# Kernel optimization log

Measured on AMD Instinct MI355X. Metric: run time of the kernel, lower is better.

Reference implementation:

```python
import jax, jax.numpy as jnp
import numpy as np

B, S, I, HS = 256, 512, 64, 128


def setup_inputs() -> dict:
    key = jax.random.key(0)
    ks = jax.random.split(key, 5)
    def xavier(k, shape):
        fan_in, fan_out = shape
        lim = float(np.sqrt(6.0 / (fan_in + fan_out)))
        return jax.random.uniform(k, shape, jnp.float32, -lim, lim)
    return {
        "x": jax.random.normal(ks[0], (B, S, I), jnp.float32),
        "TimeDiff": jax.random.uniform(ks[1], (B, S, I), jnp.float32),
        "weights_x": xavier(ks[2], (I, 5 * HS)),
        "weights_h": xavier(ks[3], (HS, 3 * HS)),
        "weights_t": xavier(ks[4], (I, 3 * HS)),
        "bias": jnp.zeros((5 * HS,), jnp.float32),
    }


def _time_lstm(x, TimeDiff, weights_x, weights_h, weights_t, bias):
    hs = weights_h.shape[0]
    bs = x.shape[0]
    # the original clamps weights_t[:, :HS] to max=0 in-place every step;
    # clamping once up front is equivalent.
    wt = weights_t.at[:, :hs].set(jnp.minimum(weights_t[:, :hs], 0.0))
    # precompute input-dependent projections for the whole sequence
    gx = jnp.einsum('bsi,ih->bsh', x, weights_x)        # (B,S,5H)
    gt = jnp.einsum('bsi,ih->bsh', TimeDiff, wt)         # (B,S,3H)

    b0, b1, b2, b3, b4 = (bias[:hs], bias[hs:2*hs], bias[2*hs:3*hs],
                          bias[3*hs:4*hs], bias[4*hs:])

    def step(carry, inp):
        h, c = carry
        gx_t, gt_t = inp                                  # (B,5H), (B,3H)
        xh = h @ weights_h                                # (B,3H)
        i_t = jax.nn.sigmoid(gx_t[:, :hs] + xh[:, :hs] + b0)
        t1 = jax.nn.sigmoid(gx_t[:, hs:2*hs] + jnp.tanh(gt_t[:, :hs]) + b1)
        t2 = jax.nn.sigmoid(gx_t[:, 2*hs:3*hs] + jnp.tanh(gt_t[:, hs:2*hs]) + b2)
        cwa = jnp.tanh(gx_t[:, 3*hs:4*hs] + xh[:, hs:2*hs] + b3)
        c_tilde = jax.nn.sigmoid((1.0 - i_t * t1) * c + i_t * t1 * cwa)
        c_new = jax.nn.sigmoid((1.0 - i_t) * c + i_t * t2 * cwa)
        o_t = jax.nn.sigmoid(gx_t[:, 4*hs:] + gt_t[:, 2*hs:] + xh[:, 2*hs:] + b4)
        h_new = o_t + jnp.tanh(c_tilde)
        return (h_new, c_new), h_new

    h0 = jnp.zeros((bs, hs), x.dtype)
    c0 = jnp.zeros((bs, hs), x.dtype)
    # scan over time: (S,B,*)
    (h_f, c_f), hseq = jax.lax.scan(
        step, (h0, c0),
        (jnp.swapaxes(gx, 0, 1), jnp.swapaxes(gt, 0, 1)))
    hidden_seq = jnp.swapaxes(hseq, 0, 1)                 # (B,S,H)
    return hidden_seq, (h_f, c_f)


def reference(x, TimeDiff, weights_x, weights_h, weights_t, bias):
    return _time_lstm(x, TimeDiff, weights_x, weights_h, weights_t, bias)
```

## Files before the change

kernel.cpp:

```cpp
#include <hip/hip_runtime.h>

typedef unsigned short ushort_t;
typedef unsigned int uint_t;
typedef short short8 __attribute__((ext_vector_type(8)));
typedef float f32x4 __attribute__((ext_vector_type(4)));
typedef uint_t u32x2 __attribute__((ext_vector_type(2)));
typedef _Float16 half2_t __attribute__((ext_vector_type(2)));

__device__ __forceinline__ float sigm(float x) { return 1.f / (1.f + __expf(-x)); }
__device__ __forceinline__ float tanh_s(float x) {
  float e = __expf(2.f * fabsf(x));
  float r = 1.f - 2.f / (e + 1.f);
  return copysignf(r, x);
}
__device__ __forceinline__ float dot2h(half2_t a, half2_t b, float c) {
#if __has_builtin(__builtin_amdgcn_fdot2)
  return __builtin_amdgcn_fdot2(a, b, c, false);
#else
  return c + (float)a.x * (float)b.x + (float)a.y * (float)b.y;
#endif
}
__device__ __forceinline__ uint_t cvtpk_bf16(float a, float b) {
  uint_t r;
  asm("v_cvt_pk_bf16_f32 %0, %1, %2" : "=v"(r) : "v"(a), "v"(b));
  return r;
}
__device__ __forceinline__ short8 ld_cvt8(const float* p) {
  f32x4 v0 = *(const f32x4*)p;
  f32x4 v1 = *(const f32x4*)(p + 4);
  union { short8 s; uint_t u[4]; } r;
  r.u[0] = cvtpk_bf16(v0[0], v0[1]);
  r.u[1] = cvtpk_bf16(v0[2], v0[3]);
  r.u[2] = cvtpk_bf16(v1[0], v1[1]);
  r.u[3] = cvtpk_bf16(v1[2], v1[3]);
  return r.s;
}
__device__ __forceinline__ float f16b2f(uint_t bits) {
  union { ushort_t s; _Float16 h; } v; v.s = (ushort_t)bits; return (float)v.h;
}
__device__ __forceinline__ uint_t f2f16b(float f) {
  union { _Float16 h; ushort_t s; } v; v.h = (_Float16)f; return v.s;
}

#define MFMAB(a, b, c) __builtin_amdgcn_mfma_f32_16x16x32_bf16((a), (b), (c), 0, 0, 0)

__global__ __launch_bounds__(512) void gemm_g(
    const float* __restrict__ x, const float* __restrict__ td,
    const float* __restrict__ wx, const float* __restrict__ wt,
    const float* __restrict__ bias, u32x2* __restrict__ G,
    int t0, int TC, int ltc, int rpt)
{
  const int tid = threadIdx.x;
  const int wv = tid >> 6, lane = tid & 63;
  const int l15 = lane & 15, lg = lane >> 4;
  const int jj = wv * 16 + l15;

  short8 Bx[5][2], Bt[3][2];
#pragma unroll
  for (int s = 0; s < 5; ++s)
#pragma unroll
    for (int f = 0; f < 2; ++f) {
      const float* wp = wx + (size_t)(f * 32 + lg * 8) * 640 + s * 128 + jj;
      union { short8 v; uint_t u[4]; } r;
#pragma unroll
      for (int q = 0; q < 4; ++q)
        r.u[q] = cvtpk_bf16(wp[(2 * q) * 640], wp[(2 * q + 1) * 640]);
      Bx[s][f] = r.v;
    }
#pragma unroll
  for (int s = 0; s < 3; ++s)
#pragma unroll
    for (int f = 0; f < 2; ++f) {
      const float* wp = wt + (size_t)(f * 32 + lg * 8) * 384 + s * 128 + jj;
      union { short8 v; uint_t u[4]; } r;
#pragma unroll
      for (int q = 0; q < 4; ++q) {
        float w0 = wp[(2 * q) * 384], w1 = wp[(2 * q + 1) * 384];
        if (s == 0) { w0 = fminf(w0, 0.f); w1 = fminf(w1, 0.f); }
        r.u[q] = cvtpk_bf16(w0, w1);
      }
      Bt[s][f] = r.v;
    }

  const float b0f = bias[jj], b1f = bias[128 + jj], b2f = bias[256 + jj];
  const float b3f = bias[384 + jj], b4f = bias[512 + jj];

#pragma unroll 1
  for (int it = 0; it < rpt; ++it) {
    const int m0 = (blockIdx.x * rpt + it) * 16;
    const int m = m0 + l15;
    const int bb = m >> ltc, tt = m & (TC - 1);
    const size_t ro = ((size_t)(bb * 512) + t0 + tt) * 64 + lg * 8;
    short8 xa0 = ld_cvt8(x + ro), xa1 = ld_cvt8(x + ro + 32);
    short8 ta0 = ld_cvt8(td + ro), ta1 = ld_cvt8(td + ro + 32);

    f32x4 g0{}, g1{}, g2{}, g3{}, g4{}, q0{}, q1{}, q2{};
    g0 = MFMAB(xa0, Bx[0][0], g0); g0 = MFMAB(xa1, Bx[0][1], g0);
    g1 = MFMAB(xa0, Bx[1][0], g1); g1 = MFMAB(xa1, Bx[1][1], g1);
    g2 = MFMAB(xa0, Bx[2][0], g2); g2 = MFMAB(xa1, Bx[2][1], g2);
    g3 = MFMAB(xa0, Bx[3][0], g3); g3 = MFMAB(xa1, Bx[3][1], g3);
    g4 = MFMAB(xa0, Bx[4][0], g4); g4 = MFMAB(xa1, Bx[4][1], g4);
    q0 = MFMAB(ta0, Bt[0][0], q0); q0 = MFMAB(ta1, Bt[0][1], q0);
    q1 = MFMAB(ta0, Bt[1][0], q1); q1 = MFMAB(ta1, Bt[1][1], q1);
    q2 = MFMAB(ta0, Bt[2][0], q2); q2 = MFMAB(ta1, Bt[2][1], q2);

#pragma unroll
    for (int r = 0; r < 4; ++r) {
      float v0 = g0[r] + b0f;
      float T1 = sigm(g1[r] + b1f + tanh_s(q0[r]));
      float T2 = sigm(g2[r] + b2f + tanh_s(q1[r]));
      float v3 = g3[r] + b3f;
      float v4 = g4[r] + b4f + q2[r];
      uint_t t1u = (uint_t)(T1 * 255.f + 0.5f);
      uint_t t2u = (uint_t)(T2 * 255.f + 0.5f);
      u32x2 P;
      P[0] = f2f16b(v0) | (f2f16b(v3) << 16);
      P[1] = f2f16b(v4) | (t1u << 16) | (t2u << 24);
      G[(size_t)(m0 + lg * 4 + r) * 128 + jj] = P;
    }
  }
}

__global__ __launch_bounds__(768) void scan_k(
    const u32x2* __restrict__ G, const float* __restrict__ wh,
    float* __restrict__ out, float* __restrict__ sh, float* __restrict__ sc,
    int t0, int t1, int TC)
{
  __shared__ __attribute__((aligned(16))) _Float16 h_lds[128];
  __shared__ float xh_lds[768];
  const int tid = threadIdx.x;
  const int b = blockIdx.x;
  const int half = (tid >= 384) ? 1 : 0;
  const int j = tid - half * 384;

  half2_t w2[32];
  {
    const float* wp = wh + (size_t)(half * 64) * 384 + j;
#pragma unroll
    for (int k = 0; k < 32; ++k)
      w2[k] = half2_t{(_Float16)wp[(2 * k) * 384], (_Float16)wp[(2 * k + 1) * 384]};
  }

  float c_last = 0.f, h0v = 0.f;
  if (tid < 128) {
    if (t0 > 0) { h0v = sh[b * 128 + tid]; c_last = sc[b * 128 + tid]; }
    h_lds[tid] = (_Float16)h0v;
  }
  float h_last = h0v;

  const u32x2* Gp = G + (size_t)b * TC * 128 + (tid & 127);
  float* outp = out + (size_t)b * 65536 + tid;

  u32x2 p0{}, p1{}, p2{}, p3{};
  if (tid < 128) {
    p0 = Gp[0];
    p1 = Gp[128];
    p2 = Gp[256];
    p3 = Gp[384];
  }
  __syncthreads();

#define SCAN_STEP(P, TABS)                                                   \
  {                                                                          \
       \
    u32x2 cur = P;                                                           \
    if (tid < 128) {                                                         \
      int ldr = (TABS) - t0 + 4; if (ldr > TC - 1) ldr = TC - 1;             \
      P = Gp[(size_t)ldr * 128];                                             \
    }                                                                        \
    float a0 = 0.f, a1 = 0.f, a2 = 0.f, a3 = 0.f;                            \
    const short8* hv8 = ((const short8*)h_lds) + half * 8;                   \
    _Pragma("unroll")                                                        \
    for (int kk = 0; kk < 8; ++kk) {                                         \
      union { short8 s; half2_t h[4]; } u; u.s = hv8[kk];                    \
      a0 = dot2h(u.h[0], w2[kk * 4 + 0], a0);                                \
      a1 = dot2h(u.h[1], w2[kk * 4 + 1], a1);                                \
      a2 = dot2h(u.h[2], w2[kk * 4 + 2], a2);                                \
      a3 = dot2h(u.h[3], w2[kk * 4 + 3], a3);                                \
    }                                                                        \
    xh_lds[tid] = (a0 + a1) + (a2 + a3);                                     \
    asm volatile("s_waitcnt lgkmcnt(0)" ::: "memory");                       \
    __builtin_amdgcn_s_barrier();                                            \
    if (tid < 128) {                                                         \
      float xh0 = xh_lds[tid] + xh_lds[tid + 384];                           \
      float xh1 = xh_lds[tid + 128] + xh_lds[tid + 512];                     \
      float xh2 = xh_lds[tid + 256] + xh_lds[tid + 640];                     \
      uint_t lo = cur[0], hi = cur[1];                                       \
      float g0v = f16b2f(lo & 0xffffu), g3v = f16b2f(lo >> 16);              \
      float g4v = f16b2f(hi & 0xffffu);                                      \
      float T1 = (float)((hi >> 16) & 255u) * (1.f / 255.f);                 \
      float T2 = (float)(hi >> 24) * (1.f / 255.f);                          \
      float i_t = sigm(g0v + xh0);                                           \
      float it1 = i_t * T1;                                                  \
      float cwa = tanh_s(g3v + xh1);                                         \
      float ctl = sigm((1.f - it1) * c_last + it1 * cwa);                    \
      float cnw = sigm((1.f - i_t) * c_last + i_t * T2 * cwa);               \
      float o_t = sigm(g4v + xh2);                                           \
      float hn = o_t + tanh_s(ctl);                                          \
      outp[(size_t)(TABS) * 128] = hn;                                       \
      h_lds[tid] = (_Float16)hn;                                             \
      c_last = cnw; h_last = hn;                                             \
    }                                                                        \
    asm volatile("s_waitcnt lgkmcnt(0)" ::: "memory");                       \
    __builtin_amdgcn_s_barrier();                                            \
  }

  for (int t = t0; t < t1; t += 4) {
    SCAN_STEP(p0, t);
    SCAN_STEP(p1, t + 1);
    SCAN_STEP(p2, t + 2);
    SCAN_STEP(p3, t + 3);
  }
#undef SCAN_STEP

  if (tid < 128) {
    if (t1 == 512) {
      out[(size_t)16777216 + b * 128 + tid] = h_last;
      out[(size_t)16777216 + 32768 + b * 128 + tid] = c_last;
    } else {
      sh[b * 128 + tid] = h_last;
      sc[b * 128 + tid] = c_last;
    }
  }
}

extern "C" void kernel_launch(void* const* d_in, const int* in_sizes, int n_in,
                              void* d_out, int out_size, void* d_ws, size_t ws_size,
                              hipStream_t stream) {
  const float* x    = (const float*)d_in[0];
  const float* td   = (const float*)d_in[1];
  const float* wx   = (const float*)d_in[2];
  const float* wh   = (const float*)d_in[3];
  const float* wt   = (const float*)d_in[4];
  const float* bias = (const float*)d_in[5];
  float* out = (float*)d_out;

  int TC = 512;
  while (TC > 16 && (size_t)256 * TC * 128 * 8 + 262144 > ws_size) TC >>= 1;
  int ltc = 0; while ((1 << ltc) < TC) ++ltc;

  u32x2* G = (u32x2*)d_ws;
  float* sh = (float*)((char*)d_ws + (size_t)256 * TC * 128 * 8);
  float* sc = sh + 256 * 128;

  const int rpt = 16;
  const int gblocks = (256 * TC / 16) / rpt;

  for (int t0 = 0; t0 < 512; t0 += TC) {
    gemm_g<<<gblocks, 512, 0, stream>>>(x, td, wx, wt, bias, G, t0, TC, ltc, rpt);
    scan_k<<<256, 768, 0, stream>>>(G, wh, out, sh, sc, t0, t0 + TC, TC);
  }
}
```

Before: 449.7 us.

## Collapse scan block to 128 threads each computing full 3-gate recurrent dot

The recurrent scan kernel shrinks from 768 threads per batch row (split-K across two halves with an LDS reduction) to 128 threads. Each thread now holds all three gate columns of W_h in registers (192 half2 values) and computes the full K=128 dot product. h is double-buffered in LDS so each step needs only one barrier, and the cross-thread xh reduction through LDS is gone. The trade-off is roughly six times more serial dot work per thread and heavy register pressure (possible spills), in exchange for fewer barriers and less synchronisation traffic.

```diff
diff --git a/kernel.cpp b/kernel.cpp
--- a/kernel.cpp
+++ b/kernel.cpp
@@ -4,6 +4,7 @@
 typedef unsigned int uint_t;
 typedef short short8 __attribute__((ext_vector_type(8)));
 typedef float f32x4 __attribute__((ext_vector_type(4)));
+typedef float f32x2 __attribute__((ext_vector_type(2)));
 typedef uint_t u32x2 __attribute__((ext_vector_type(2)));
 typedef _Float16 half2_t __attribute__((ext_vector_type(2)));
 
@@ -121,106 +122,97 @@
   }
 }
 
-__global__ __launch_bounds__(768) void scan_k(
+__global__ __launch_bounds__(128, 1) void scan_k(
     const u32x2* __restrict__ G, const float* __restrict__ wh,
     float* __restrict__ out, float* __restrict__ sh, float* __restrict__ sc,
     int t0, int t1, int TC)
 {
-  __shared__ __attribute__((aligned(16))) _Float16 h_lds[128];
-  __shared__ float xh_lds[768];
-  const int tid = threadIdx.x;
+  __shared__ __attribute__((aligned(16))) _Float16 h_lds[2][128];
+  const int j = threadIdx.x;
   const int b = blockIdx.x;
-  const int half = (tid >= 384) ? 1 : 0;
-  const int j = tid - half * 384;
-
-  half2_t w2[32];
-  {
-    const float* wp = wh + (size_t)(half * 64) * 384 + j;
-#pragma unroll
-    for (int k = 0; k < 32; ++k)
-      w2[k] = half2_t{(_Float16)wp[(2 * k) * 384], (_Float16)wp[(2 * k + 1) * 384]};
+
+  half2_t w2[3][64];
+#pragma unroll
+  for (int s = 0; s < 3; ++s) {
+    const float* wp = wh + s * 128 + j;
+#pragma unroll
+    for (int k = 0; k < 64; ++k)
+      w2[s][k] = half2_t{(_Float16)wp[(size_t)(2 * k) * 384],
+                         (_Float16)wp[(size_t)(2 * k + 1) * 384]};
   }
 
   float c_last = 0.f, h0v = 0.f;
-  if (tid < 128) {
-    if (t0 > 0) { h0v = sh[b * 128 + tid]; c_last = sc[b * 128 + tid]; }
-    h_lds[tid] = (_Float16)h0v;
-  }
+  if (t0 > 0) { h0v = sh[b * 128 + j]; c_last = sc[b * 128 + j]; }
   float h_last = h0v;
-
-  const u32x2* Gp = G + (size_t)b * TC * 128 + (tid & 127);
-  float* outp = out + (size_t)b * 65536 + tid;
-
-  u32x2 p0{}, p1{}, p2{}, p3{};
-  if (tid < 128) {
-    p0 = Gp[0];
-    p1 = Gp[128];
-    p2 = Gp[256];
-    p3 = Gp[384];
-  }
+  h_lds[0][j] = (_Float16)h0v;
+
+  const u32x2* Gp = G + (size_t)b * TC * 128 + j;
+  float* outp = out + (size_t)b * 65536 + j;
+
+  u32x2 p0 = Gp[0], p1 = Gp[128], p2 = Gp[256], p3 = Gp[384];
   __syncthreads();
 
-#define SCAN_STEP(P, TABS)                                                   \
+#define SCAN_STEP(P, TT, CUR, NXT)                                           \
   {                                                                          \
-       \
     u32x2 cur = P;                                                           \
-    if (tid < 128) {                                                         \
-      int ldr = (TABS) - t0 + 4; if (ldr > TC - 1) ldr = TC - 1;             \
-      P = Gp[(size_t)ldr * 128];                                             \
+    int tp = (TT) + 4; if (tp > TC - 1) tp = TC - 1;                         \
+    P = Gp[(size_t)tp * 128];                                                \
+    float a0=0.f,a1=0.f,a2=0.f,a3=0.f;                                       \
+    float d0=0.f,d1=0.f,d2=0.f,d3=0.f;                                       \
+    float e0=0.f,e1=0.f,e2=0.f,e3=0.f;                                       \
+    const short8* hv8 = (const short8*)h_lds[CUR];                           \
+    _Pragma("unroll")                                                        \
+    for (int kk = 0; kk < 16; ++kk) {                                        \
+      union { short8 s; half2_t h[4]; } u; u.s = hv8[kk];                    \
+      a0 = dot2h(u.h[0], w2[0][kk * 4 + 0], a0);                             \
+      a1 = dot2h(u.h[1], w2[0][kk * 4 + 1], a1);                             \
+      a2 = dot2h(u.h[2], w2[0][kk * 4 + 2], a2);                             \
+      a3 = dot2h(u.h[3], w2[0][kk * 4 + 3], a3);                             \
+      d0 = dot2h(u.h[0], w2[1][kk * 4 + 0], d0);                             \
+      d1 = dot2h(u.h[1], w2[1][kk * 4 + 1], d1);                             \
+      d2 = dot2h(u.h[2], w2[1][kk * 4 + 2], d2);                             \
+      d3 = dot2h(u.h[3], w2[1][kk * 4 + 3], d3);                             \
+      e0 = dot2h(u.h[0], w2[2][kk * 4 + 0], e0);                             \
+      e1 = dot2h(u.h[1], w2[2][kk * 4 + 1], e1);                             \
+      e2 = dot2h(u.h[2], w2[2][kk * 4 + 2], e2);                             \
+      e3 = dot2h(u.h[3], w2[2][kk * 4 + 3], e3);                             \
     }                                                                        \
-    float a0 = 0.f, a1 = 0.f, a2 = 0.f, a3 = 0.f;                            \
-    const short8* hv8 = ((const short8*)h_lds) + half * 8;                   \
-    _Pragma("unroll")                                                        \
-    for (int kk = 0; kk < 8; ++kk) {                                         \
-      union { short8 s; half2_t h[4]; } u; u.s = hv8[kk];                    \
-      a0 = dot2h(u.h[0], w2[kk * 4 + 0], a0);                                \
-      a1 = dot2h(u.h[1], w2[kk * 4 + 1], a1);                                \
-      a2 = dot2h(u.h[2], w2[kk * 4 + 2], a2);                                \
-      a3 = dot2h(u.h[3], w2[kk * 4 + 3], a3);                                \
-    }                                                                        \
-    xh_lds[tid] = (a0 + a1) + (a2 + a3);                                     \
+    float xh0 = (a0 + a1) + (a2 + a3);                                       \
+    float xh1 = (d0 + d1) + (d2 + d3);                                       \
+    float xh2 = (e0 + e1) + (e2 + e3);                                       \
+    uint_t lo = cur[0], hi = cur[1];                                         \
+    float g0v = f16b2f(lo & 0xffffu), g3v = f16b2f(lo >> 16);                \
+    float g4v = f16b2f(hi & 0xffffu);                                        \
+    float T1 = (float)((hi >> 16) & 255u) * (1.f / 255.f);                   \
+    float T2 = (float)(hi >> 24) * (1.f / 255.f);                            \
+    float i_t = sigm(g0v + xh0);                                             \
+    float it1 = i_t * T1;                                                    \
+    float cwa = tanh_s(g3v + xh1);                                           \
+    float ctl = sigm((1.f - it1) * c_last + it1 * cwa);                      \
+    float cnw = sigm((1.f - i_t) * c_last + i_t * T2 * cwa);                 \
+    float o_t = sigm(g4v + xh2);                                             \
+    float hn = o_t + tanh_s(ctl);                                            \
+    h_lds[NXT][j] = (_Float16)hn;                                            \
+    outp[(size_t)(t0 + (TT)) * 128] = hn;                                    \
+    c_last = cnw; h_last = hn;                                               \
     asm volatile("s_waitcnt lgkmcnt(0)" ::: "memory");                       \
     __builtin_amdgcn_s_barrier();                                            \
-    if (tid < 128) {                                                         \
-      float xh0 = xh_lds[tid] + xh_lds[tid + 384];                           \
-      float xh1 = xh_lds[tid + 128] + xh_lds[tid + 512];                     \
-      float xh2 = xh_lds[tid + 256] + xh_lds[tid + 640];                     \
-      uint_t lo = cur[0], hi = cur[1];                                       \
-      float g0v = f16b2f(lo & 0xffffu), g3v = f16b2f(lo >> 16);              \
-      float g4v = f16b2f(hi & 0xffffu);                                      \
-      float T1 = (float)((hi >> 16) & 255u) * (1.f / 255.f);                 \
-      float T2 = (float)(hi >> 24) * (1.f / 255.f);                          \
-      float i_t = sigm(g0v + xh0);                                           \
-      float it1 = i_t * T1;                                                  \
-      float cwa = tanh_s(g3v + xh1);                                         \
-      float ctl = sigm((1.f - it1) * c_last + it1 * cwa);                    \
-      float cnw = sigm((1.f - i_t) * c_last + i_t * T2 * cwa);               \
-      float o_t = sigm(g4v + xh2);                                           \
-      float hn = o_t + tanh_s(ctl);                                          \
-      outp[(size_t)(TABS) * 128] = hn;                                       \
-      h_lds[tid] = (_Float16)hn;                                             \
-      c_last = cnw; h_last = hn;                                             \
-    }                                                                        \
-    asm volatile("s_waitcnt lgkmcnt(0)" ::: "memory");                       \
-    __builtin_amdgcn_s_barrier();                                            \
-  }
-
-  for (int t = t0; t < t1; t += 4) {
-    SCAN_STEP(p0, t);
-    SCAN_STEP(p1, t + 1);
-    SCAN_STEP(p2, t + 2);
-    SCAN_STEP(p3, t + 3);
+  }
+
+  for (int tt = 0; tt < TC; tt += 4) {
+    SCAN_STEP(p0, tt, 0, 1);
+    SCAN_STEP(p1, tt + 1, 1, 0);
+    SCAN_STEP(p2, tt + 2, 0, 1);
+    SCAN_STEP(p3, tt + 3, 1, 0);
   }
 #undef SCAN_STEP
 
-  if (tid < 128) {
-    if (t1 == 512) {
-      out[(size_t)16777216 + b * 128 + tid] = h_last;
-      out[(size_t)16777216 + 32768 + b * 128 + tid] = c_last;
-    } else {
-      sh[b * 128 + tid] = h_last;
-      sc[b * 128 + tid] = c_last;
-    }
+  if (t1 == 512) {
+    out[(size_t)16777216 + b * 128 + j] = h_last;
+    out[(size_t)16777216 + 32768 + b * 128 + j] = c_last;
+  } else {
+    sh[b * 128 + j] = h_last;
+    sc[b * 128 + j] = c_last;
   }
 }
 
@@ -248,6 +240,6 @@
 
   for (int t0 = 0; t0 < 512; t0 += TC) {
     gemm_g<<<gblocks, 512, 0, stream>>>(x, td, wx, wt, bias, G, t0, TC, ltc, rpt);
-    scan_k<<<256, 768, 0, stream>>>(G, wh, out, sh, sc, t0, t0 + TC, TC);
-  }
-}
+    scan_k<<<256, 128, 0, stream>>>(G, wh, out, sh, sc, t0, t0 + TC, TC);
+  }
+}
```

Result: slower. 573.7 us (+27.6%).
